# Optimization experiments

Hardware: AMD Instinct MI355X
Metric: run time of the kernel (lower is better)

## Reference

```python
import jax, jax.numpy as jnp
import numpy as np

N, E, F_IN, H, G, K = 50000, 800000, 64, 200, 256, 3


def setup_inputs() -> dict:
    key = jax.random.key(0)
    ks = jax.random.split(key, 12)
    x = jax.random.normal(ks[0], (N, F_IN), jnp.float32)
    edge_index = jax.random.randint(ks[1], (2, E), 0, N, dtype=jnp.int64)
    batch = jnp.sort(jax.random.randint(ks[2], (N,), 0, G, dtype=jnp.int64))
    lmax = 1.5 + jax.random.uniform(ks[3], (G,), jnp.float32)  # per-graph lambda_max

    def lin(k, i, o):
        return (jax.random.normal(k, (K, i, o), jnp.float32) / np.sqrt(i)).astype(jnp.float32)

    return dict(
        x=x, edge_index=edge_index, batch=batch, lmax=lmax,
        W1=lin(ks[4], F_IN, H), b1=jnp.zeros((H,), jnp.float32),
        W2=lin(ks[5], H, H),    b2=jnp.zeros((H,), jnp.float32),
        W3=lin(ks[6], H, H),    b3=jnp.zeros((H,), jnp.float32),
        W4=lin(ks[7], H, H),    b4=jnp.zeros((H,), jnp.float32),
        fc_w=(jax.random.normal(ks[8], (2 * H, 2), jnp.float32) / np.sqrt(2 * H)).astype(jnp.float32),
        fc_b=jnp.zeros((2,), jnp.float32),
    )


def reference(x, edge_index, batch, lmax, W1, b1, W2, b2, W3, b3, W4, b4, fc_w, fc_b):
    n = x.shape[0]
    g = lmax.shape[0]
    src, dst = edge_index[0], edge_index[1]

    # PyG ChebConv sym normalization: L_hat = 2/lambda_max * (I - D^-1/2 A D^-1/2) - I
    deg = jax.ops.segment_sum(jnp.ones(src.shape[0], x.dtype), src, num_segments=n)
    dis = jnp.where(deg > 0, jnp.maximum(deg, 1.0) ** -0.5, 0.0)  # deg^{-1/2}, inf -> 0
    scale = 2.0 / lmax                                            # [G]
    w = -dis[src] * dis[dst] * scale[batch[src]]                  # off-diagonal edge weights [E]
    diag = scale[batch] - 1.0                                     # diagonal of L_hat, [N]

    def prop(h):  # L_hat @ h via sparse scatter
        return jax.ops.segment_sum(w[:, None] * h[src], dst, num_segments=n) + diag[:, None] * h

    def cheb(h, W, b):  # K=3 Chebyshev recurrence
        Tx0 = h
        Tx1 = prop(h)
        Tx2 = 2.0 * prop(Tx1) - Tx0
        return Tx0 @ W[0] + Tx1 @ W[1] + Tx2 @ W[2] + b

    h = jax.nn.relu(cheb(x, W1, b1))
    h = jax.nn.relu(cheb(h, W2, b2))
    h = jax.nn.relu(cheb(h, W3, b3))
    h = jax.nn.relu(cheb(h, W4, b4))

    cnt = jax.ops.segment_sum(jnp.ones(n, h.dtype), batch, num_segments=g)
    pooled_mean = jax.ops.segment_sum(h, batch, num_segments=g) / jnp.maximum(cnt, 1.0)[:, None]
    pooled_max = jax.ops.segment_max(h, batch, num_segments=g)
    z = jnp.concatenate([pooled_mean, pooled_max], axis=1) @ fc_w + fc_b
    return jax.nn.log_softmax(z, axis=1)
```

## Files before the change

### kernel.cpp

```cpp
#include <hip/hip_runtime.h>
#include <math.h>

#define NN 50000
#define MP 50048
#define NE 800000
#define FIN 64
#define HD 200
#define NG 256
#define SCAN_B 256
#define KPAD 224
#define NT 13
#define HB 12544
#define PER_B 3125

typedef _Float16 h16;
typedef __attribute__((ext_vector_type(8))) _Float16 half8;
typedef __attribute__((ext_vector_type(4))) float float4v;
typedef unsigned long long u64;

__global__ __launch_bounds__(256) void k_hist(const int* __restrict__ src,
                                              const int* __restrict__ dst,
                                              unsigned* __restrict__ pSrc,
                                              unsigned* __restrict__ pDst, int E) {
    __shared__ unsigned h[HB];
    int tid = threadIdx.x;
    int isDst = blockIdx.x >> 8;
    int b = blockIdx.x & 255;
    const int* idx = isDst ? dst : src;
    unsigned* partial = isDst ? pDst : pSrc;
    int e0 = b * PER_B;
    int v[13];
#pragma unroll
    for (int j = 0; j < 13; ++j) {
        int o = j * 256 + tid;
        v[j] = (o < PER_B) ? idx[e0 + o] : -1;
    }
#pragma unroll
    for (int pass = 0; pass < 2; ++pass) {
        for (int t = tid; t < HB; t += 256) h[t] = 0;
        __syncthreads();
        int lo = pass * (2 * HB);
#pragma unroll
        for (int j = 0; j < 13; ++j) {
            int vv = v[j] - lo;
            if (vv >= 0 && vv < 2 * HB)
                atomicAdd(&h[vv >> 1], (vv & 1) ? 0x10000u : 1u);
        }
        __syncthreads();
        unsigned* pb = partial + ((size_t)pass * 256 + b) * HB;
        for (int t = tid; t < HB; t += 256) pb[t] = h[t];
        __syncthreads();
    }
}

__global__ void k_hredscan(const unsigned* __restrict__ pSrc, unsigned* __restrict__ pDst,
                           int* __restrict__ degi, int* __restrict__ cntd, int n) {
    int i = blockIdx.x * blockDim.x + threadIdx.x;
    if (i < 2 * HB) {
        int pass = i / HB, p = i - pass * HB;
        const unsigned* pb = pSrc + (size_t)pass * 256 * HB + p;
        unsigned s = 0;
        for (int b = 0; b < 256; ++b) s += pb[(size_t)b * HB];
        int n0 = pass * 2 * HB + 2 * p;
        if (n0 < n)     degi[n0]     = (int)(s & 0xffffu);
        if (n0 + 1 < n) degi[n0 + 1] = (int)(s >> 16);
    } else if (i < 4 * HB) {
        int j = i - 2 * HB;
        int pass = j / HB, p = j - pass * HB;
        unsigned* pb = pDst + (size_t)pass * 256 * HB + p;
        unsigned run = 0;
        for (int b = 0; b < 256; ++b) {
            unsigned c = pb[(size_t)b * HB];
            pb[(size_t)b * HB] = run;
            run += c;
        }
        int n0 = pass * 2 * HB + 2 * p;
        if (n0 < n)     cntd[n0]     = (int)(run & 0xffffu);
        if (n0 + 1 < n) cntd[n0 + 1] = (int)(run >> 16);
    }
}

__global__ void k_prep(const int* __restrict__ degi, const int* __restrict__ batch,
                       const float* __restrict__ lmax, float* __restrict__ dis,
                       float* __restrict__ qs, float* __restrict__ diag,
                       int* __restrict__ gstart, int n, int gN) {
    int b = blockIdx.x;
    if (b < gN) {
        int i = b * 256 + threadIdx.x;
        if (i < n) {
            int d = degi[i];
            float di = (d > 0) ? (1.0f / sqrtf((float)d)) : 0.0f;
            float sc = 2.0f / lmax[batch[i]];
            dis[i] = di;
            qs[i] = -di * sc;
            diag[i] = sc - 1.0f;
        }
    } else {
        int g = (b - gN) * 256 + threadIdx.x;
        if (g > NG) return;
        if (g == NG) { gstart[NG] = n; return; }
        int lo = 0, hi = n;
        while (lo < hi) {
            int mid = (lo + hi) >> 1;
            if (batch[mid] < g) lo = mid + 1; else hi = mid;
        }
        gstart[g] = lo;
    }
}

__global__ void k_scan1(const int* __restrict__ cnt, int* __restrict__ excl,
                        int* __restrict__ bsum, int n) {
    __shared__ int sh[SCAN_B];
    int tid = threadIdx.x;
    int i = blockIdx.x * SCAN_B + tid;
    int v = (i < n) ? cnt[i] : 0;
    sh[tid] = v;
    __syncthreads();
    for (int off = 1; off < SCAN_B; off <<= 1) {
        int t = (tid >= off) ? sh[tid - off] : 0;
        __syncthreads();
        sh[tid] += t;
        __syncthreads();
    }
    if (i < n) excl[i] = sh[tid] - v;
    if (tid == SCAN_B - 1) bsum[blockIdx.x] = sh[tid];
}

__global__ void k_scan2(int* __restrict__ bsum, int nb) {
    __shared__ int sh[SCAN_B];
    int tid = threadIdx.x;
    int v = (tid < nb) ? bsum[tid] : 0;
    sh[tid] = v;
    __syncthreads();
    for (int off = 1; off < SCAN_B; off <<= 1) {
        int t = (tid >= off) ? sh[tid - off] : 0;
        __syncthreads();
        sh[tid] += t;
        __syncthreads();
    }
    if (tid < nb) bsum[tid] = sh[tid] - v;
}

__global__ void k_meta(const int* __restrict__ excl, const int* __restrict__ bsum,
                       const int* __restrict__ cntd, const float* __restrict__ diag,
                       u64* __restrict__ meta, int n) {
    int i = blockIdx.x * 256 + threadIdx.x;
    if (i >= n) return;
    unsigned start = (unsigned)(excl[i] + bsum[i >> 8]);
    union { h16 h; unsigned short u; } d;
    d.h = (h16)diag[i];
    meta[i] = (u64)start | ((u64)(unsigned)cntd[i] << 32) | ((u64)d.u << 48);
}

__global__ __launch_bounds__(256) void k_fillcsr2(
    const int* __restrict__ src, const int* __restrict__ dst,
    const float* __restrict__ qs, const float* __restrict__ dis,
    const int* __restrict__ excl, const int* __restrict__ bsum,
    const unsigned* __restrict__ hpart, unsigned* __restrict__ csr, int E) {
    __shared__ unsigned lrank[HB];
    int tid = threadIdx.x;
    int e0 = blockIdx.x * PER_B;
    int vs[13], vd[13];
#pragma unroll
    for (int j = 0; j < 13; ++j) {
        int o = j * 256 + tid;
        vs[j] = (o < PER_B) ? src[e0 + o] : -1;
        vd[j] = (o < PER_B) ? dst[e0 + o] : -1;
    }
#pragma unroll
    for (int pass = 0; pass < 2; ++pass) {
        for (int t = tid; t < HB; t += 256) lrank[t] = 0;
        __syncthreads();
        int lo = pass * (2 * HB);
        const unsigned* base = hpart + ((size_t)pass * 256 + blockIdx.x) * HB;
#pragma unroll
        for (int j = 0; j < 13; ++j) {
            int vv = vd[j] - lo;
            if (vv >= 0 && vv < 2 * HB) {
                unsigned old = atomicAdd(&lrank[vv >> 1], (vv & 1) ? 0x10000u : 1u);
                unsigned rank = (vv & 1) ? (old >> 16) : (old & 0xffffu);
                unsigned bs = base[vv >> 1];
                unsigned bb = (vv & 1) ? (bs >> 16) : (bs & 0xffffu);
                int s = vs[j], d = vd[j];
                int pos = excl[d] + bsum[d >> 8] + (int)bb + (int)rank;
                union { h16 h; unsigned short u; } cw;
                cw.h = (h16)(qs[s] * dis[d]);
                csr[pos] = (unsigned)s | ((unsigned)cw.u << 16);
            }
        }
        __syncthreads();
    }
}

__global__ void k_wprep(const float* __restrict__ W1, const float* __restrict__ W2,
                        const float* __restrict__ W3, const float* __restrict__ W4,
                        h16* __restrict__ wt0, h16* __restrict__ wt1,
                        h16* __restrict__ wt2, h16* __restrict__ wt3,
                        const float* __restrict__ x, h16* __restrict__ x16,
                        h16* __restrict__ hi0) {
    const int T0 = 3 * 2 * 208 * 32, T = 3 * 7 * 208 * 32;
    const int TW = T0 + 3 * T;
    int idx = blockIdx.x * blockDim.x + threadIdx.x;
    if (idx >= TW) {
        int i = idx - TW;
        if (i < NN * FIN) { x16[i] = (h16)x[i]; return; }
        int i2 = i - NN * FIN;
        if (i2 < MP * 24) {
            int row = i2 / 24;
            hi0[(size_t)row * KPAD + 200 + (i2 - row * 24)] = (h16)0.f;
        }
        return;
    }
    const float* W; h16* o; int fin, ksteps, li;
    if (idx < T0) { W = W1; o = wt0; fin = FIN; ksteps = 2; li = idx; }
    else {
        int r = idx - T0; int l = r / T;
        li = r - l * T; fin = HD; ksteps = 7;
        W = (l == 0) ? W2 : ((l == 1) ? W3 : W4);
        o = (l == 0) ? wt1 : ((l == 1) ? wt2 : wt3);
    }
    int kk = li & 31;
    int r2 = li >> 5;
    int nn = r2 % 208;
    int r3 = r2 / 208;
    int ks = r3 % ksteps;
    int seg = r3 / ksteps;
    int k = ks * 32 + kk;
    float val = 0.f;
    if (nn < HD && k < fin) {
        size_t base = (size_t)k * HD + nn;
        size_t segsz = (size_t)fin * HD;
        if (seg == 0)      val = W[base] - W[2 * segsz + base];
        else if (seg == 1) val = W[segsz + base];
        else               val = 2.f * W[2 * segsz + base];
    }
    o[li] = (h16)val;
}

__global__ __launch_bounds__(256) void k_gather(
    const u64* __restrict__ meta, const unsigned* __restrict__ csr,
    const h16* __restrict__ hin16, h16* __restrict__ hout16,
    int s16, int lsh, int n) {
    int per = 256 >> lsh;
    int i = blockIdx.x * per + (threadIdx.x >> lsh);
    if (i >= n) return;
    int lane = threadIdx.x & ((1 << lsh) - 1);
    int c0 = lane * 4;
    if (c0 >= s16) return;
    unsigned su = (unsigned)s16;
    union U { uint2 u; h16 h[4]; };
    union W16 { unsigned short u; h16 h; };
    u64 m = __builtin_nontemporal_load(&meta[i]);
    int start = (int)(unsigned)(m & 0xffffffffu);
    int cnt = (int)((m >> 32) & 0xffffu);
    W16 dg16; dg16.u = (unsigned short)(m >> 48);
    float dg = (float)dg16.h;
    const unsigned* cp = csr + start;
    float g0 = 0.f, g1 = 0.f, g2 = 0.f, g3 = 0.f;
    int k = 0;
    for (; k + 7 < cnt; k += 8) {
        unsigned e[8];
#pragma unroll
        for (int j = 0; j < 8; ++j) e[j] = __builtin_nontemporal_load(&cp[k + j]);
        U p[8];
#pragma unroll
        for (int j = 0; j < 8; ++j)
            p[j].u = *(const uint2*)(hin16 + (size_t)((e[j] & 0xffffu) * su + (unsigned)c0));
#pragma unroll
        for (int j = 0; j < 8; ++j) {
            W16 wv; wv.u = (unsigned short)(e[j] >> 16);
            float w = (float)wv.h;
            g0 += w * (float)p[j].h[0];
            g1 += w * (float)p[j].h[1];
            g2 += w * (float)p[j].h[2];
            g3 += w * (float)p[j].h[3];
        }
    }
    for (; k + 1 < cnt; k += 2) {
        unsigned e0 = __builtin_nontemporal_load(&cp[k]);
        unsigned e1 = __builtin_nontemporal_load(&cp[k + 1]);
        U p0, p1;
        p0.u = *(const uint2*)(hin16 + (size_t)((e0 & 0xffffu) * su + (unsigned)c0));
        p1.u = *(const uint2*)(hin16 + (size_t)((e1 & 0xffffu) * su + (unsigned)c0));
        W16 w0v, w1v; w0v.u = (unsigned short)(e0 >> 16); w1v.u = (unsigned short)(e1 >> 16);
        float w0 = (float)w0v.h, w1 = (float)w1v.h;
        g0 += w0 * (float)p0.h[0] + w1 * (float)p1.h[0];
        g1 += w0 * (float)p0.h[1] + w1 * (float)p1.h[1];
        g2 += w0 * (float)p0.h[2] + w1 * (float)p1.h[2];
        g3 += w0 * (float)p0.h[3] + w1 * (float)p1.h[3];
    }
    if (k < cnt) {
        unsigned e0 = __builtin_nontemporal_load(&cp[k]);
        U p0;
        p0.u = *(const uint2*)(hin16 + (size_t)((e0 & 0xffffu) * su + (unsigned)c0));
        W16 w0v; w0v.u = (unsigned short)(e0 >> 16);
        float w0 = (float)w0v.h;
        g0 += w0 * (float)p0.h[0];
        g1 += w0 * (float)p0.h[1];
        g2 += w0 * (float)p0.h[2];
        g3 += w0 * (float)p0.h[3];
    }
    U hs; hs.u = *(const uint2*)(hin16 + (size_t)((unsigned)i * su + (unsigned)c0));
    U o;
    o.h[0] = (h16)(g0 + dg * (float)hs.h[0]);
    o.h[1] = (h16)(g1 + dg * (float)hs.h[1]);
    o.h[2] = (h16)(g2 + dg * (float)hs.h[2]);
    o.h[3] = (h16)(g3 + dg * (float)hs.h[3]);
    *(uint2*)(hout16 + (size_t)((unsigned)i * su + (unsigned)c0)) = o.u;
}

__global__ __launch_bounds__(256) void k_gemm16(
    const h16* __restrict__ A0, const h16* __restrict__ A1, const h16* __restrict__ A2,
    int strideA, int ksteps,
    const h16* __restrict__ Wt, const float* __restrict__ bias,
    h16* __restrict__ out16, int n) {
    int tid = threadIdx.x;
    int wave = tid >> 6, lane = tid & 63;
    int nq = lane & 15, quad = lane >> 4;
    int row0 = (blockIdx.x * 4 + wave) * 32;
    const h16* Aseg[3] = {A0, A1, A2};

    float4v acc[2][NT];
#pragma unroll
    for (int r = 0; r < 2; r++)
#pragma unroll
        for (int t = 0; t < NT; t++) acc[r][t] = (float4v)0.f;

    for (int seg = 0; seg < 3; ++seg) {
        const h16* Ab = Aseg[seg] + (size_t)(row0 + nq) * strideA + quad * 8;
        const h16* Bb = Wt + (size_t)seg * ksteps * 208 * 32 + (size_t)nq * 32 + quad * 8;
        for (int ks = 0; ks < ksteps; ++ks) {
            half8 af0 = *(const half8*)(Ab + ks * 32);
            half8 af1 = *(const half8*)(Ab + 16 * strideA + ks * 32);
            const h16* Bk = Bb + (size_t)ks * 208 * 32;
#pragma unroll
            for (int t = 0; t < NT; ++t) {
                half8 bf = *(const half8*)(Bk + t * 16 * 32);
                acc[0][t] = __builtin_amdgcn_mfma_f32_16x16x32_f16(af0, bf, acc[0][t], 0, 0, 0);
                acc[1][t] = __builtin_amdgcn_mfma_f32_16x16x32_f16(af1, bf, acc[1][t], 0, 0, 0);
            }
        }
    }
#pragma unroll
    for (int r = 0; r < 2; ++r) {
        int rowb = row0 + r * 16 + quad * 4;
#pragma unroll
        for (int t = 0; t < NT; ++t) {
            int col = t * 16 + nq;
            if (col >= HD) continue;
            float bj = bias[col];
#pragma unroll
            for (int g = 0; g < 4; ++g) {
                int row = rowb + g;
                if (row < n)
                    out16[(size_t)row * KPAD + col] = (h16)fmaxf(acc[r][t][g] + bj, 0.0f);
            }
        }
    }
}

__global__ __launch_bounds__(256) void k_pool_fc(
    const h16* __restrict__ Hf, const int* __restrict__ gstart,
    const float* __restrict__ fcw, const float* __restrict__ fcb,
    float* __restrict__ out) {
    __shared__ float red[8];
    int g = blockIdx.x;
    int j = threadIdx.x;
    int i0 = gstart[g], i1 = gstart[g + 1];
    float s0 = 0.f, s1 = 0.f, s2 = 0.f, s3 = 0.f, mx = 0.f;
    if (j < HD) {
        int i = i0;
        for (; i + 3 < i1; i += 4) {
            float v0 = (float)Hf[(size_t)i * KPAD + j];
            float v1 = (float)Hf[(size_t)(i + 1) * KPAD + j];
            float v2 = (float)Hf[(size_t)(i + 2) * KPAD + j];
            float v3 = (float)Hf[(size_t)(i + 3) * KPAD + j];
            s0 += v0; s1 += v1; s2 += v2; s3 += v3;
            mx = fmaxf(mx, fmaxf(fmaxf(v0, v1), fmaxf(v2, v3)));
        }
        for (; i < i1; ++i) {
            float v = (float)Hf[(size_t)i * KPAD + j];
            s0 += v; mx = fmaxf(mx, v);
        }
    }
    float cntf = (float)(i1 - i0);
    float mean = (s0 + s1 + s2 + s3) / fmaxf(cntf, 1.f);
    float p0 = 0.f, p1 = 0.f;
    if (j < HD) {
        p0 = mean * fcw[2 * j]     + mx * fcw[2 * (HD + j)];
        p1 = mean * fcw[2 * j + 1] + mx * fcw[2 * (HD + j) + 1];
    }
#pragma unroll
    for (int o = 32; o > 0; o >>= 1) {
        p0 += __shfl_down(p0, o);
        p1 += __shfl_down(p1, o);
    }
    int wave = j >> 6, lane = j & 63;
    if (lane == 0) { red[wave * 2] = p0; red[wave * 2 + 1] = p1; }
    __syncthreads();
    if (j == 0) {
        float z0 = red[0] + red[2] + red[4] + red[6] + fcb[0];
        float z1 = red[1] + red[3] + red[5] + red[7] + fcb[1];
        float m = fmaxf(z0, z1);
        float lse = m + logf(expf(z0 - m) + expf(z1 - m));
        out[g * 2 + 0] = z0 - lse;
        out[g * 2 + 1] = z1 - lse;
    }
}

extern "C" void kernel_launch(void* const* d_in, const int* in_sizes, int n_in,
                              void* d_out, int out_size, void* d_ws, size_t ws_size,
                              hipStream_t stream) {
    const float* x     = (const float*)d_in[0];
    const int*   edge  = (const int*)d_in[1];
    const int*   batch = (const int*)d_in[2];
    const float* lmax  = (const float*)d_in[3];
    const float* W1 = (const float*)d_in[4];  const float* b1 = (const float*)d_in[5];
    const float* W2 = (const float*)d_in[6];  const float* b2 = (const float*)d_in[7];
    const float* W3 = (const float*)d_in[8];  const float* b3 = (const float*)d_in[9];
    const float* W4 = (const float*)d_in[10]; const float* b4 = (const float*)d_in[11];
    const float* fcw = (const float*)d_in[12]; const float* fcb = (const float*)d_in[13];
    float* out = (float*)d_out;

    const int n = NN, E = NE;
    const int* src = edge;
    const int* dst = edge + E;

    float* ws = (float*)d_ws;
    size_t off = 0;
    auto alloc = [&](size_t nfloats) { float* p = ws + off; off += (nfloats + 3) & ~(size_t)3; return p; };
    int*   degi   = (int*)alloc(NN);
    float* dis    = alloc(NN);
    float* qs     = alloc(NN);
    float* diag   = alloc(NN);
    int*   cntd   = (int*)alloc(NN);
    int*   excl   = (int*)alloc(NN);
    int*   bsum   = (int*)alloc(SCAN_B);
    unsigned* csr = (unsigned*)alloc(NE);
    u64*   meta   = (u64*)alloc((size_t)2 * NN);
    int*   gstart = (int*)alloc(NG + 1);
    unsigned* pSrc = (unsigned*)alloc((size_t)2 * 256 * HB);
    unsigned* pDst = (unsigned*)alloc((size_t)2 * 256 * HB);
    h16*   x16    = (h16*)alloc((size_t)MP * FIN / 2);
    h16*   hi0    = (h16*)alloc((size_t)MP * KPAD / 2);
    h16*   hi1    = (h16*)alloc((size_t)MP * KPAD / 2);
    h16*   hi2    = (h16*)alloc((size_t)MP * KPAD / 2);
    const int WSZ0 = 3 * 2 * 208 * 32;
    const int WSZ  = 3 * 7 * 208 * 32;
    h16* wt0 = (h16*)alloc(WSZ0 / 2);
    h16* wt1 = (h16*)alloc(WSZ / 2);
    h16* wt2 = (h16*)alloc(WSZ / 2);
    h16* wt3 = (h16*)alloc(WSZ / 2);

    dim3 blk(256);
    int gN = (n + 255) / 256;
    int gScan = (n + SCAN_B - 1) / SCAN_B;
    int gGemm = MP / 128;
    int gWp = (WSZ0 + 3 * WSZ + NN * FIN + MP * 24 + 255) / 256;

    k_wprep<<<gWp, blk, 0, stream>>>(W1, W2, W3, W4, wt0, wt1, wt2, wt3, x, x16, hi0);
    k_hist<<<512, blk, 0, stream>>>(src, dst, pSrc, pDst, E);
    k_hredscan<<<(4 * HB + 255) / 256, blk, 0, stream>>>(pSrc, pDst, degi, cntd, n);
    k_prep<<<gN + 2, blk, 0, stream>>>(degi, batch, lmax, dis, qs, diag, gstart, n, gN);
    k_scan1<<<gScan, blk, 0, stream>>>(cntd, excl, bsum, n);
    k_scan2<<<1, blk, 0, stream>>>(bsum, gScan);
    k_meta<<<gScan, blk, 0, stream>>>(excl, bsum, cntd, diag, meta, n);
    k_fillcsr2<<<256, blk, 0, stream>>>(src, dst, qs, dis, excl, bsum, pDst, csr, E);

    const h16* wt[4] = {wt0, wt1, wt2, wt3};
    const float* bl[4] = {b1, b2, b3, b4};
    for (int l = 0; l < 4; l++) {
        int s16 = (l == 0) ? FIN : KPAD;
        int lsh = (l == 0) ? 4 : 6;
        int per = 256 >> lsh;
        int gGat = (n + per - 1) / per;
        int ksteps = (l == 0) ? 2 : 7;
        const h16* a0 = (l == 0) ? x16 : hi0;
        k_gather<<<gGat, blk, 0, stream>>>(meta, csr, a0, hi1, s16, lsh, n);
        k_gather<<<gGat, blk, 0, stream>>>(meta, csr, hi1, hi2, s16, lsh, n);
        k_gemm16<<<gGemm, blk, 0, stream>>>(a0, hi1, hi2, s16, ksteps, wt[l], bl[l],
                                            (l < 3) ? hi0 : hi1, n);
    }

    k_pool_fc<<<NG, blk, 0, stream>>>(hi1, gstart, fcw, fcb, out);
}
```

Measured before the change: 775.0 us.

## Add XCC-aware column-group gather with atomic chunk scheduling for last layer

Adds a persistent gather kernel that reads the hardware XCC id and assigns each chiplet a 32-column feature slice. Blocks pull 64-node chunks from per-column-group atomic counters. The aim is to keep each XCC's L2 working set to one column slice of the input features, improving cache reuse of the random neighbor reads, and to balance load dynamically. It is used only for layer 4 and adds atomic scheduling overhead, extra syncthreads, and a counter reset inside the prep kernel.

```diff
diff --git a/kernel.cpp b/kernel.cpp
--- a/kernel.cpp
+++ b/kernel.cpp
@@ -12,6 +12,7 @@
 #define NT 13
 #define HB 12544
 #define PER_B 3125
+#define GCH 64
 
 typedef _Float16 h16;
 typedef __attribute__((ext_vector_type(8))) _Float16 half8;
@@ -83,7 +84,8 @@
 __global__ void k_prep(const int* __restrict__ degi, const int* __restrict__ batch,
                        const float* __restrict__ lmax, float* __restrict__ dis,
                        float* __restrict__ qs, float* __restrict__ diag,
-                       int* __restrict__ gstart, int n, int gN) {
+                       int* __restrict__ gstart, unsigned* __restrict__ ctr,
+                       int n, int gN) {
     int b = blockIdx.x;
     if (b < gN) {
         int i = b * 256 + threadIdx.x;
@@ -95,6 +97,8 @@
             qs[i] = -di * sc;
             diag[i] = sc - 1.0f;
         }
+    } else if (b == gN + 2) {
+        if (threadIdx.x < 64) ctr[threadIdx.x] = 0u;
     } else {
         int g = (b - gN) * 256 + threadIdx.x;
         if (g > NG) return;
@@ -309,6 +313,96 @@
     *(uint2*)(hout16 + (size_t)((unsigned)i * su + (unsigned)c0)) = o.u;
 }
 
+__global__ __launch_bounds__(256) void k_gatherx(
+    const u64* __restrict__ meta, const unsigned* __restrict__ csr,
+    const h16* __restrict__ hin16, h16* __restrict__ hout16,
+    unsigned* __restrict__ ctr, int s16, int n, int ncg) {
+    unsigned xcc;
+    asm volatile("s_getreg_b32 %0, hwreg(HW_REG_XCC_ID, 0, 4)" : "=s"(xcc));
+    int g0 = (int)(xcc % (unsigned)ncg);
+    int tid = threadIdx.x;
+    int sub = tid >> 3;
+    int lane = tid & 7;
+    unsigned su = (unsigned)s16;
+    int nch = (n + GCH - 1) / GCH;
+    __shared__ int sch;
+    union U { uint2 u; u64 q; h16 h[4]; };
+    union W16 { unsigned short u; h16 h; };
+    for (int t = 0; t < ncg; ++t) {
+        int g = g0 + t; if (g >= ncg) g -= ncg;
+        unsigned c0 = (unsigned)(g * 32 + lane * 4);
+        for (;;) {
+            __syncthreads();
+            if (tid == 0) sch = (int)atomicAdd(&ctr[g], 1u);
+            __syncthreads();
+            int ch = sch;
+            if (ch >= nch) break;
+#pragma unroll
+            for (int p = 0; p < GCH / 32; ++p) {
+                int i = ch * GCH + p * 32 + sub;
+                if (i >= n) continue;
+                u64 m = __builtin_nontemporal_load(&meta[i]);
+                int start = (int)(unsigned)(m & 0xffffffffu);
+                int cnt = (int)((m >> 32) & 0xffffu);
+                W16 dg16; dg16.u = (unsigned short)(m >> 48);
+                float dg = (float)dg16.h;
+                const unsigned* cp = csr + start;
+                float g0v = 0.f, g1v = 0.f, g2v = 0.f, g3v = 0.f;
+                int k = 0;
+                for (; k + 7 < cnt; k += 8) {
+                    unsigned e[8];
+#pragma unroll
+                    for (int j = 0; j < 8; ++j) e[j] = __builtin_nontemporal_load(&cp[k + j]);
+                    U pr[8];
+#pragma unroll
+                    for (int j = 0; j < 8; ++j)
+                        pr[j].u = *(const uint2*)(hin16 + (size_t)((e[j] & 0xffffu) * su + c0));
+#pragma unroll
+                    for (int j = 0; j < 8; ++j) {
+                        W16 wv; wv.u = (unsigned short)(e[j] >> 16);
+                        float w = (float)wv.h;
+                        g0v += w * (float)pr[j].h[0];
+                        g1v += w * (float)pr[j].h[1];
+                        g2v += w * (float)pr[j].h[2];
+                        g3v += w * (float)pr[j].h[3];
+                    }
+                }
+                for (; k + 1 < cnt; k += 2) {
+                    unsigned e0 = __builtin_nontemporal_load(&cp[k]);
+                    unsigned e1 = __builtin_nontemporal_load(&cp[k + 1]);
+                    U p0, p1;
+                    p0.u = *(const uint2*)(hin16 + (size_t)((e0 & 0xffffu) * su + c0));
+                    p1.u = *(const uint2*)(hin16 + (size_t)((e1 & 0xffffu) * su + c0));
+                    W16 w0v, w1v; w0v.u = (unsigned short)(e0 >> 16); w1v.u = (unsigned short)(e1 >> 16);
+                    float w0 = (float)w0v.h, w1 = (float)w1v.h;
+                    g0v += w0 * (float)p0.h[0] + w1 * (float)p1.h[0];
+                    g1v += w0 * (float)p0.h[1] + w1 * (float)p1.h[1];
+                    g2v += w0 * (float)p0.h[2] + w1 * (float)p1.h[2];
+                    g3v += w0 * (float)p0.h[3] + w1 * (float)p1.h[3];
+                }
+                if (k < cnt) {
+                    unsigned e0 = __builtin_nontemporal_load(&cp[k]);
+                    U p0;
+                    p0.u = *(const uint2*)(hin16 + (size_t)((e0 & 0xffffu) * su + c0));
+                    W16 w0v; w0v.u = (unsigned short)(e0 >> 16);
+                    float w0 = (float)w0v.h;
+                    g0v += w0 * (float)p0.h[0];
+                    g1v += w0 * (float)p0.h[1];
+                    g2v += w0 * (float)p0.h[2];
+                    g3v += w0 * (float)p0.h[3];
+                }
+                U hs; hs.u = *(const uint2*)(hin16 + (size_t)((unsigned)i * su + c0));
+                U o;
+                o.h[0] = (h16)(g0v + dg * (float)hs.h[0]);
+                o.h[1] = (h16)(g1v + dg * (float)hs.h[1]);
+                o.h[2] = (h16)(g2v + dg * (float)hs.h[2]);
+                o.h[3] = (h16)(g3v + dg * (float)hs.h[3]);
+                __builtin_nontemporal_store(o.q, (u64*)(hout16 + (size_t)((unsigned)i * su + c0)));
+            }
+        }
+    }
+}
+
 __global__ __launch_bounds__(256) void k_gemm16(
     const h16* __restrict__ A0, const h16* __restrict__ A1, const h16* __restrict__ A2,
     int strideA, int ksteps,
@@ -438,6 +532,7 @@
     int*   bsum   = (int*)alloc(SCAN_B);
     unsigned* csr = (unsigned*)alloc(NE);
     u64*   meta   = (u64*)alloc((size_t)2 * NN);
+    unsigned* ctr = (unsigned*)alloc(64);
     int*   gstart = (int*)alloc(NG + 1);
     unsigned* pSrc = (unsigned*)alloc((size_t)2 * 256 * HB);
     unsigned* pDst = (unsigned*)alloc((size_t)2 * 256 * HB);
@@ -461,7 +556,7 @@
     k_wprep<<<gWp, blk, 0, stream>>>(W1, W2, W3, W4, wt0, wt1, wt2, wt3, x, x16, hi0);
     k_hist<<<512, blk, 0, stream>>>(src, dst, pSrc, pDst, E);
     k_hredscan<<<(4 * HB + 255) / 256, blk, 0, stream>>>(pSrc, pDst, degi, cntd, n);
-    k_prep<<<gN + 2, blk, 0, stream>>>(degi, batch, lmax, dis, qs, diag, gstart, n, gN);
+    k_prep<<<gN + 3, blk, 0, stream>>>(degi, batch, lmax, dis, qs, diag, gstart, ctr, n, gN);
     k_scan1<<<gScan, blk, 0, stream>>>(cntd, excl, bsum, n);
     k_scan2<<<1, blk, 0, stream>>>(bsum, gScan);
     k_meta<<<gScan, blk, 0, stream>>>(excl, bsum, cntd, diag, meta, n);
@@ -471,13 +566,18 @@
     const float* bl[4] = {b1, b2, b3, b4};
     for (int l = 0; l < 4; l++) {
         int s16 = (l == 0) ? FIN : KPAD;
-        int lsh = (l == 0) ? 4 : 6;
-        int per = 256 >> lsh;
-        int gGat = (n + per - 1) / per;
         int ksteps = (l == 0) ? 2 : 7;
         const h16* a0 = (l == 0) ? x16 : hi0;
-        k_gather<<<gGat, blk, 0, stream>>>(meta, csr, a0, hi1, s16, lsh, n);
-        k_gather<<<gGat, blk, 0, stream>>>(meta, csr, hi1, hi2, s16, lsh, n);
+        if (l < 3) {
+            int lsh = (l == 0) ? 4 : 6;
+            int per = 256 >> lsh;
+            int gGat = (n + per - 1) / per;
+            k_gather<<<gGat, blk, 0, stream>>>(meta, csr, a0, hi1, s16, lsh, n);
+            k_gather<<<gGat, blk, 0, stream>>>(meta, csr, hi1, hi2, s16, lsh, n);
+        } else {
+            k_gatherx<<<2048, blk, 0, stream>>>(meta, csr, a0, hi1, ctr + 0, s16, n, 7);
+            k_gatherx<<<2048, blk, 0, stream>>>(meta, csr, hi1, hi2, ctr + 8, s16, n, 7);
+        }
         k_gemm16<<<gGemm, blk, 0, stream>>>(a0, hi1, hi2, s16, ksteps, wt[l], bl[l],
                                             (l < 3) ? hi0 : hi1, n);
     }
```

After: 1.212 ms. 56.3% more time.
